# Kernel optimization log

Hardware: AMD Instinct MI355X
Metric: run time of the kernel (lower is better)

The kernel has to match this reference:

```python
import jax, jax.numpy as jnp
import numpy as np

B, C, F, T = 4, 64, 256, 256
CH = C // 2  # self.n_ch inside the module
EPS = 1e-5


def _cbp(x, W, b, g, be, m, v, a):
    # 1x1 conv == channel matmul, then BatchNorm (inference stats) + PReLU (scalar slope)
    y = jnp.einsum('oi,bift->boft', W, x) + b[None, :, None, None]
    y = (y - m[None, :, None, None]) * jax.lax.rsqrt(v[None, :, None, None] + EPS)
    y = y * g[None, :, None, None] + be[None, :, None, None]
    return jnp.where(y > 0, y, a * y)


def setup_inputs() -> dict:
    key = jax.random.key(0)
    ks = jax.random.split(key, 16)

    def conv_params(i, cin, cout, pre):
        W = jax.random.normal(ks[i], (cout, cin), dtype=jnp.float32) * 0.05
        return {
            pre + '_W': W,
            pre + '_b': jnp.zeros((cout,), jnp.float32),
            pre + '_g': jnp.ones((cout,), jnp.float32),
            pre + '_be': jnp.zeros((cout,), jnp.float32),
            pre + '_m': jax.random.normal(ks[i + 1], (cout,), dtype=jnp.float32) * 0.1,
            pre + '_v': jax.random.uniform(ks[i + 2], (cout,), dtype=jnp.float32) + 0.5,
            pre + '_a': jnp.float32(0.25),
        }

    d = {
        'inp': jax.random.normal(ks[12], (B, C, F, T), dtype=jnp.float32),
        'x': jax.random.normal(ks[13], (B, C, F, T), dtype=jnp.float32),
    }
    d.update(conv_params(0, C, 2 * CH, 'fqk'))
    d.update(conv_params(3, C, CH, 'fv'))
    d.update(conv_params(6, C, 2 * CH, 'tqk'))
    d.update(conv_params(9, CH, C, 'proj'))
    return d


def reference(inp, x,
              fqk_W, fqk_b, fqk_g, fqk_be, fqk_m, fqk_v, fqk_a,
              fv_W, fv_b, fv_g, fv_be, fv_m, fv_v, fv_a,
              tqk_W, tqk_b, tqk_g, tqk_be, tqk_m, tqk_v, tqk_a,
              proj_W, proj_b, proj_g, proj_be, proj_m, proj_v, proj_a):
    scale = 1.0 / jnp.sqrt(jnp.float32(CH))

    # frequency attention
    f_qk = _cbp(inp, fqk_W, fqk_b, fqk_g, fqk_be, fqk_m, fqk_v, fqk_a)  # B,2CH,F,T
    vf = _cbp(x, fv_W, fv_b, fv_g, fv_be, fv_m, fv_v, fv_a)             # B,CH,F,T
    r = f_qk.reshape(f_qk.shape[0], CH, 2, F, T)  # 'b (c k) f t -> b c k f t'
    qf, kf = r[:, :, 0], r[:, :, 1]
    f_score = jnp.einsum('bcft,bcyt->btfy', qf, kf) * scale
    f_score = jax.nn.softmax(f_score, axis=-1)
    fout = jnp.einsum('btfy,bcyt->bcft', f_score, vf)

    # time attention (causal mask)
    t_qk = _cbp(inp, tqk_W, tqk_b, tqk_g, tqk_be, tqk_m, tqk_v, tqk_a)
    r = t_qk.reshape(t_qk.shape[0], CH, 2, F, T)
    qt, kt = r[:, :, 0], r[:, :, 1]
    t_score = jnp.einsum('bcft,bcfy->bfty', qt, kt) * scale
    mask = jnp.triu(jnp.ones((T, T), dtype=bool), k=1)  # j - i + 1 with i == j
    neg = -jnp.finfo(t_score.dtype).max
    t_score = jnp.where(mask, neg, t_score)
    t_score = jax.nn.softmax(t_score, axis=-1)
    tout = jnp.einsum('bfty,bcfy->bcft', t_score, fout)

    out = _cbp(tout, proj_W, proj_b, proj_g, proj_be, proj_m, proj_v, proj_a)
    return out + x
```

## Files before the change

kernel.cpp:

```cpp
#include <hip/hip_runtime.h>
#include <hip/hip_bf16.h>

typedef __hip_bfloat16 bf16;
typedef __attribute__((ext_vector_type(8))) short bf16x8;
typedef __attribute__((ext_vector_type(4))) float f32x4;
typedef __attribute__((ext_vector_type(16))) float f32x16;
typedef __attribute__((ext_vector_type(8))) unsigned short u16x8;
typedef __attribute__((ext_vector_type(4))) unsigned int u32x4;
typedef __attribute__((ext_vector_type(2))) unsigned int u32x2;

struct ConvP {
  const float* W; const float* bi; const float* g; const float* be;
  const float* m; const float* v; const float* a;
};

#define QS (0.17677669529663687f * 1.4426950408889634f)

__device__ __forceinline__ unsigned short f2bf(float f) {
  __hip_bfloat16 h = __float2bfloat16(f);
  return __builtin_bit_cast(unsigned short, h);
}
__device__ __forceinline__ float bf2f(unsigned short u) {
  return __uint_as_float(((unsigned)u) << 16);
}
__device__ __forceinline__ float fast_exp2(float x) {
#if __has_builtin(__builtin_amdgcn_exp2f)
  return __builtin_amdgcn_exp2f(x);
#else
  return exp2f(x);
#endif
}

__global__ __launch_bounds__(256, 2) void conv_qkv(
    const float* __restrict__ inp, const float* __restrict__ x,
    ConvP fqk, ConvP fv, ConvP tqk,
    bf16* __restrict__ Qf, bf16* __restrict__ Kf, bf16* __restrict__ Vf,
    bf16* __restrict__ Qt, bf16* __restrict__ Kt)
{
  __shared__ __attribute__((aligned(16))) unsigned short Xb[64 * 260];
  __shared__ __attribute__((aligned(16))) unsigned short S0[256 * 40];
  __shared__ __attribute__((aligned(16))) unsigned short S1[256 * 40];
  __shared__ __attribute__((aligned(8)))  float2 Pc[160];

  const int tid = threadIdx.x;
  const int b = blockIdx.x >> 8;
  const int f = blockIdx.x & 255;
  const size_t gbase = (size_t)b * 64 * 65536 + f * 256;
  const size_t tbase = (size_t)(b * 256 + f) * 8192;

  const int lane = tid & 63;
  const int wid = tid >> 6;
  const int m16 = lane & 15;
  const int quad = lane >> 4;

  if (tid < 160) {
    const ConvP& P = (tid < 64) ? fqk : (tid < 128) ? tqk : fv;
    const int o = (tid < 64) ? tid : (tid < 128) ? tid - 64 : tid - 128;
    float A = P.g[o] * rsqrtf(P.v[o] + 1e-5f);
    float B2 = (P.bi[o] - P.m[o]) * A + P.be[o];
    if (tid < 128 && ((o & 1) == 0)) { A *= QS; B2 *= QS; }
    Pc[tid] = make_float2(A, B2);
  }

  auto load_X = [&](const float* __restrict__ src) {
    #pragma unroll
    for (int r = 0; r < 16; ++r) {
      const int idx = r * 256 + tid;
      const int c = idx >> 6;
      const int t0 = (idx & 63) * 4;
      const float4 v = *(const float4*)(src + gbase + (size_t)c * 65536 + t0);
      unsigned lo = (unsigned)f2bf(v.x) | (((unsigned)f2bf(v.y)) << 16);
      unsigned hi = (unsigned)f2bf(v.z) | (((unsigned)f2bf(v.w)) << 16);
      u32x2 pk = {lo, hi};
      *(u32x2*)&Xb[c * 260 + t0] = pk;
    }
  };

  auto load_A = [&](const float* __restrict__ W, int rowbase, int ks) {
    const float* p = W + (rowbase + m16) * 64 + ks * 32 + quad * 8;
    const float4 lo = *(const float4*)p;
    const float4 hi = *(const float4*)(p + 4);
    bf16x8 r;
    r[0] = (short)f2bf(lo.x); r[1] = (short)f2bf(lo.y);
    r[2] = (short)f2bf(lo.z); r[3] = (short)f2bf(lo.w);
    r[4] = (short)f2bf(hi.x); r[5] = (short)f2bf(hi.y);
    r[6] = (short)f2bf(hi.z); r[7] = (short)f2bf(hi.w);
    return r;
  };

  auto load_B = [&](int tt, int ks) {
    const int t = tt * 16 + m16;
    const int i0 = ks * 32 + quad * 8;
    bf16x8 r;
    #pragma unroll
    for (int j = 0; j < 8; ++j) r[j] = (short)Xb[(i0 + j) * 260 + t];
    return r;
  };

  auto emit = [&](const unsigned short* S, bf16* __restrict__ dst) {
    #pragma unroll
    for (int r = 0; r < 4; ++r) {
      const int chunk = r * 256 + tid;
      const int t = chunk >> 2, part = chunk & 3;
      u32x4 v = *(const u32x4*)&S[t * 40 + part * 8];
      *(u32x4*)(dst + tbase + (size_t)chunk * 8) = v;
    }
  };

  auto leaky = [](float y, float alpha) { return y > 0.f ? y : alpha * y; };

  auto qk_pass = [&](const ConvP& P, int pcb, const bf16x8 (&Bf)[4][2]) {
    bf16x8 A[4][2];
    #pragma unroll
    for (int ot = 0; ot < 4; ++ot)
      #pragma unroll
      for (int ks = 0; ks < 2; ++ks) A[ot][ks] = load_A(P.W, ot * 16, ks);
    float pA[4][4], pB[4][4];
    #pragma unroll
    for (int ot = 0; ot < 4; ++ot)
      #pragma unroll
      for (int r = 0; r < 4; ++r) {
        const float2 pp = Pc[pcb + ot * 16 + quad * 4 + r];
        pA[ot][r] = pp.x; pB[ot][r] = pp.y;
      }
    const float alpha = P.a[0];
    #pragma unroll
    for (int i = 0; i < 4; ++i) {
      const int t = (wid * 4 + i) * 16 + m16;
      #pragma unroll
      for (int ot = 0; ot < 4; ++ot) {
        f32x4 acc = {0.f, 0.f, 0.f, 0.f};
        acc = __builtin_amdgcn_mfma_f32_16x16x32_bf16(A[ot][0], Bf[i][0], acc, 0, 0, 0);
        acc = __builtin_amdgcn_mfma_f32_16x16x32_bf16(A[ot][1], Bf[i][1], acc, 0, 0, 0);
        float y[4];
        #pragma unroll
        for (int r = 0; r < 4; ++r)
          y[r] = leaky(acc[r] * pA[ot][r] + pB[ot][r], alpha);
        const int ch0 = ot * 8 + quad * 2;
        *(unsigned*)&S0[t * 40 + ch0] = (unsigned)f2bf(y[0]) | (((unsigned)f2bf(y[2])) << 16);
        *(unsigned*)&S1[t * 40 + ch0] = (unsigned)f2bf(y[1]) | (((unsigned)f2bf(y[3])) << 16);
      }
    }
  };

  load_X(inp);
  __syncthreads();

  bf16x8 Bf[4][2];
  #pragma unroll
  for (int i = 0; i < 4; ++i)
    #pragma unroll
    for (int ks = 0; ks < 2; ++ks) Bf[i][ks] = load_B(wid * 4 + i, ks);

  qk_pass(fqk, 0, Bf);
  __syncthreads();
  emit(S0, Qf); emit(S1, Kf);
  __syncthreads();
  qk_pass(tqk, 64, Bf);
  __syncthreads();
  emit(S0, Qt); emit(S1, Kt);
  __syncthreads();
  load_X(x);
  __syncthreads();

  {
    bf16x8 A[2][2], Bv[4][2];
    #pragma unroll
    for (int i = 0; i < 4; ++i)
      #pragma unroll
      for (int ks = 0; ks < 2; ++ks) Bv[i][ks] = load_B(wid * 4 + i, ks);
    #pragma unroll
    for (int ot = 0; ot < 2; ++ot)
      #pragma unroll
      for (int ks = 0; ks < 2; ++ks) A[ot][ks] = load_A(fv.W, ot * 16, ks);
    float pA[2][4], pB[2][4];
    #pragma unroll
    for (int ot = 0; ot < 2; ++ot)
      #pragma unroll
      for (int r = 0; r < 4; ++r) {
        const float2 pp = Pc[128 + ot * 16 + quad * 4 + r];
        pA[ot][r] = pp.x; pB[ot][r] = pp.y;
      }
    const float alpha = fv.a[0];
    #pragma unroll
    for (int i = 0; i < 4; ++i) {
      const int t = (wid * 4 + i) * 16 + m16;
      #pragma unroll
      for (int ot = 0; ot < 2; ++ot) {
        f32x4 acc = {0.f, 0.f, 0.f, 0.f};
        acc = __builtin_amdgcn_mfma_f32_16x16x32_bf16(A[ot][0], Bv[i][0], acc, 0, 0, 0);
        acc = __builtin_amdgcn_mfma_f32_16x16x32_bf16(A[ot][1], Bv[i][1], acc, 0, 0, 0);
        float y[4];
        #pragma unroll
        for (int r = 0; r < 4; ++r)
          y[r] = leaky(acc[r] * pA[ot][r] + pB[ot][r], alpha);
        const int ch = ot * 16 + quad * 4;
        *(unsigned*)&S0[t * 40 + ch]     = (unsigned)f2bf(y[0]) | (((unsigned)f2bf(y[1])) << 16);
        *(unsigned*)&S0[t * 40 + ch + 2] = (unsigned)f2bf(y[2]) | (((unsigned)f2bf(y[3])) << 16);
      }
    }
  }
  __syncthreads();
  emit(S0, Vf);
}

template<bool CAUSAL>
__global__ __launch_bounds__(256, 2) void attn_k(
    const bf16* __restrict__ Qg, const bf16* __restrict__ Kg,
    const bf16* __restrict__ Vg, bf16* __restrict__ Og)
{
  __shared__ __attribute__((aligned(16))) unsigned short Kl[256 * 40];
  __shared__ __attribute__((aligned(16))) unsigned short Vt[32 * 264];
  __shared__ __attribute__((aligned(16))) unsigned short Plds[4][16 * 264];
  __shared__ __attribute__((aligned(16))) unsigned short Wsc[4][16 * 40];

  const int inst = blockIdx.x;
  const int b = inst >> 8;
  const int s = inst & 255;
  constexpr int RS = CAUSAL ? 32 : 8192;
  const int qbase = CAUSAL ? inst * 8192 : (b * 2097152 + s * 32);

  const int tid = threadIdx.x;
  #pragma unroll
  for (int k2 = 0; k2 < 4; ++k2) {
    const int chunk = k2 * 256 + tid;
    const int row = chunk >> 2, part = chunk & 3;
    u32x4 val = *(const u32x4*)(Kg + qbase + row * RS + part * 8);
    *(u32x4*)&Kl[row * 40 + part * 8] = val;
  }
  if (tid < 128) {
    const unsigned short* v0 = (const unsigned short*)(Vg + qbase) + (2 * tid) * RS;
    const unsigned short* v1 = v0 + RS;
    u16x8 a[4], c[4];
    #pragma unroll
    for (int q = 0; q < 4; ++q) {
      a[q] = *(const u16x8*)(v0 + 8 * q);
      c[q] = *(const u16x8*)(v1 + 8 * q);
    }
    unsigned int* vt32 = (unsigned int*)Vt;
    #pragma unroll
    for (int cc = 0; cc < 32; ++cc) {
      unsigned lo = a[cc >> 3][cc & 7];
      unsigned hi = c[cc >> 3][cc & 7];
      vt32[(cc * 264 + 2 * tid) >> 1] = lo | (hi << 16);
    }
  }
  __syncthreads();

  const int lane = tid & 63;
  const int wid = tid >> 6;
  const int m16 = lane & 15;
  const int quad = lane >> 4;

  unsigned short* P  = &Plds[wid][0];
  unsigned short* Ws = &Wsc[wid][0];
  const int r4 = lane >> 2, p4 = lane & 3;

  bf16x8 kfr[16];
  #pragma unroll
  for (int ct = 0; ct < 16; ++ct)
    kfr[ct] = *(const bf16x8*)&Kl[(ct * 16 + m16) * 40 + quad * 8];

  #pragma unroll 1
  for (int it = 0; it < 4; ++it) {
    const int rt = wid + 4 * it;
    {
      u32x4 qv = *(const u32x4*)(Qg + qbase + (rt * 16 + r4) * RS + p4 * 8);
      *(u32x4*)&Ws[r4 * 40 + p4 * 8] = qv;
    }
    const bf16x8 qf = *(const bf16x8*)&Ws[m16 * 40 + quad * 8];
    const int nct = CAUSAL ? (rt + 1) : 16;

    f32x4 acc[16];
    #pragma unroll
    for (int ct = 0; ct < 16; ++ct) {
      if (ct < nct) {
        f32x4 z = {0.f, 0.f, 0.f, 0.f};
        acc[ct] = __builtin_amdgcn_mfma_f32_16x16x32_bf16(qf, kfr[ct], z, 0, 0, 0);
      }
    }
    float mx[4] = {-3e38f, -3e38f, -3e38f, -3e38f};
    #pragma unroll
    for (int ct = 0; ct < 16; ++ct) if (ct < nct) {
      #pragma unroll
      for (int r = 0; r < 4; ++r) {
        float v = acc[ct][r];
        if (CAUSAL && (ct == nct - 1) && (m16 > quad * 4 + r)) v = -3e38f;
        acc[ct][r] = v;
        mx[r] = fmaxf(mx[r], v);
      }
    }
    #pragma unroll
    for (int r = 0; r < 4; ++r) {
      float m = mx[r];
      #pragma unroll
      for (int d = 1; d < 16; d <<= 1) m = fmaxf(m, __shfl_xor(m, d, 16));
      mx[r] = m;
    }
    float sum[4] = {0.f, 0.f, 0.f, 0.f};
    #pragma unroll
    for (int ct = 0; ct < 16; ++ct) if (ct < nct) {
      #pragma unroll
      for (int r = 0; r < 4; ++r) {
        float p = fast_exp2(acc[ct][r] - mx[r]);
        acc[ct][r] = p;
        sum[r] += p;
      }
    }
    float inv[4];
    #pragma unroll
    for (int r = 0; r < 4; ++r) {
      float ssum = sum[r];
      #pragma unroll
      for (int d = 1; d < 16; d <<= 1) ssum += __shfl_xor(ssum, d, 16);
      inv[r] = 1.0f / ssum;
    }
    #pragma unroll
    for (int ct = 0; ct < 16; ++ct) if (ct < nct) {
      #pragma unroll
      for (int r = 0; r < 4; ++r)
        P[(quad * 4 + r) * 264 + ct * 16 + m16] = f2bf(acc[ct][r]);
    }
    int ksteps = CAUSAL ? ((rt >> 1) + 1) : 8;
    if (CAUSAL && ((rt & 1) == 0)) {
      #pragma unroll
      for (int u = 0; u < 4; ++u) {
        const int e = lane + 64 * u;
        P[(e >> 4) * 264 + (rt + 1) * 16 + (e & 15)] = 0;
      }
    }
    f32x4 o0 = {0.f, 0.f, 0.f, 0.f}, o1 = {0.f, 0.f, 0.f, 0.f};
    #pragma unroll
    for (int ks = 0; ks < 8; ++ks) {
      if (ks < ksteps) {
        const bf16x8 pf  = *(const bf16x8*)&P[m16 * 264 + ks * 32 + quad * 8];
        const bf16x8 vf0 = *(const bf16x8*)&Vt[m16 * 264 + ks * 32 + quad * 8];
        const bf16x8 vf1 = *(const bf16x8*)&Vt[(16 + m16) * 264 + ks * 32 + quad * 8];
        o0 = __builtin_amdgcn_mfma_f32_16x16x32_bf16(pf, vf0, o0, 0, 0, 0);
        o1 = __builtin_amdgcn_mfma_f32_16x16x32_bf16(pf, vf1, o1, 0, 0, 0);
      }
    }
    #pragma unroll
    for (int r = 0; r < 4; ++r) {
      Ws[(quad * 4 + r) * 40 + m16]      = f2bf(o0[r] * inv[r]);
      Ws[(quad * 4 + r) * 40 + 16 + m16] = f2bf(o1[r] * inv[r]);
    }
    {
      u32x4 ov = *(const u32x4*)&Ws[r4 * 40 + p4 * 8];
      *(u32x4*)(Og + qbase + (rt * 16 + r4) * RS + p4 * 8) = ov;
    }
  }
}

__global__ __launch_bounds__(256) void proj_k(
    const bf16* __restrict__ tout, const float* __restrict__ x,
    ConvP pj, float* __restrict__ out)
{
  __shared__ float2 Pc[64];
  const int tid = threadIdx.x;
  const int b = blockIdx.x >> 8;
  const int f = blockIdx.x & 255;
  if (tid < 64) {
    const float A = pj.g[tid] * rsqrtf(pj.v[tid] + 1e-5f);
    const float B2 = (pj.bi[tid] - pj.m[tid]) * A + pj.be[tid];
    Pc[tid] = make_float2(A, B2);
  }
  const int lane = tid & 63;
  const int wid = tid >> 6;
  const int n32 = lane & 31;
  const int h = lane >> 5;

  bf16x8 Afr[2][2];
  #pragma unroll
  for (int ot = 0; ot < 2; ++ot)
    #pragma unroll
    for (int ks = 0; ks < 2; ++ks) {
      const float* p = pj.W + (ot * 32 + n32) * 32 + ks * 16 + h * 8;
      const float4 lo = *(const float4*)p;
      const float4 hi = *(const float4*)(p + 4);
      bf16x8 r;
      r[0] = (short)f2bf(lo.x); r[1] = (short)f2bf(lo.y);
      r[2] = (short)f2bf(lo.z); r[3] = (short)f2bf(lo.w);
      r[4] = (short)f2bf(hi.x); r[5] = (short)f2bf(hi.y);
      r[6] = (short)f2bf(hi.z); r[7] = (short)f2bf(hi.w);
      Afr[ot][ks] = r;
    }
  __syncthreads();

  const float alpha = pj.a[0];
  const size_t gbase = (size_t)b * 64 * 65536 + f * 256;
  const size_t tbase = (size_t)(b * 256 + f) * 8192;

  #pragma unroll
  for (int tt = 0; tt < 2; ++tt) {
    const int t = wid * 64 + tt * 32 + n32;
    const bf16x8 B0 = *(const bf16x8*)(tout + tbase + (size_t)t * 32 + 0 * 16 + h * 8);
    const bf16x8 B1 = *(const bf16x8*)(tout + tbase + (size_t)t * 32 + 1 * 16 + h * 8);
    #pragma unroll
    for (int ot = 0; ot < 2; ++ot) {
      f32x16 acc = {};
      acc = __builtin_amdgcn_mfma_f32_32x32x16_bf16(Afr[ot][0], B0, acc, 0, 0, 0);
      acc = __builtin_amdgcn_mfma_f32_32x32x16_bf16(Afr[ot][1], B1, acc, 0, 0, 0);
      #pragma unroll
      for (int reg = 0; reg < 16; ++reg) {
        const int o = ot * 32 + (reg & 3) + 8 * (reg >> 2) + 4 * h;
        const float2 pp = Pc[o];
        float y = acc[reg] * pp.x + pp.y;
        y = y > 0.f ? y : alpha * y;
        const size_t off = gbase + (size_t)o * 65536 + t;
        out[off] = y + x[off];
      }
    }
  }
}

extern "C" void kernel_launch(void* const* d_in, const int* in_sizes, int n_in,
                              void* d_out, int out_size, void* d_ws, size_t ws_size,
                              hipStream_t stream) {
  const float* inp = (const float*)d_in[0];
  const float* x   = (const float*)d_in[1];
  auto cp = [&](int i) {
    return ConvP{ (const float*)d_in[i],     (const float*)d_in[i + 1],
                  (const float*)d_in[i + 2], (const float*)d_in[i + 3],
                  (const float*)d_in[i + 4], (const float*)d_in[i + 5],
                  (const float*)d_in[i + 6] };
  };
  ConvP fqk = cp(2), fv = cp(9), tqk = cp(16), pj = cp(23);

  char* ws = (char*)d_ws;
  const size_t SZ = (size_t)4 * 256 * 256 * 32 * 2;
  bf16* Qf = (bf16*)(ws + 0 * SZ);
  bf16* Kf = (bf16*)(ws + 1 * SZ);
  bf16* Vf = (bf16*)(ws + 2 * SZ);
  bf16* Qt = (bf16*)(ws + 3 * SZ);
  bf16* Kt = (bf16*)(ws + 4 * SZ);
  bf16* Ft = (bf16*)(ws + 5 * SZ);
  bf16* To = (bf16*)(ws + 0 * SZ);

  conv_qkv<<<1024, 256, 0, stream>>>(inp, x, fqk, fv, tqk, Qf, Kf, Vf, Qt, Kt);
  attn_k<false><<<1024, 256, 0, stream>>>(Qf, Kf, Vf, Ft);
  attn_k<true><<<1024, 256, 0, stream>>>(Qt, Kt, Ft, To);
  proj_k<<<1024, 256, 0, stream>>>(To, x, pj, (float*)d_out);
}
```

Before: 329.9 us.

## Shrink LDS footprint to raise occupancy in conv and attention kernels

The conv kernel now splits each (b,f) row into two half-T blocks, which halves its shared-memory tiles and doubles the grid. Its launch bound is raised to 4 blocks per CU. In the attention kernel, K is stored in shared memory as an XOR-swizzled unpadded tile, and only half the K fragments are kept in registers; the rest are reloaded from shared memory. P is staged in two 128-column halves, which reuses its buffer as the Q/output scratch and drops the separate Ws array. Together these cut LDS use and register pressure so 3 blocks per CU can fit. The cost is extra LDS reads for K, more loop control, and redundant parameter setup in the conv kernel.

```diff
diff --git a/kernel.cpp b/kernel.cpp
--- a/kernel.cpp
+++ b/kernel.cpp
@@ -31,22 +31,23 @@
 #endif
 }
 
-__global__ __launch_bounds__(256, 2) void conv_qkv(
+__global__ __launch_bounds__(256, 4) void conv_qkv(
     const float* __restrict__ inp, const float* __restrict__ x,
     ConvP fqk, ConvP fv, ConvP tqk,
     bf16* __restrict__ Qf, bf16* __restrict__ Kf, bf16* __restrict__ Vf,
     bf16* __restrict__ Qt, bf16* __restrict__ Kt)
 {
-  __shared__ __attribute__((aligned(16))) unsigned short Xb[64 * 260];
-  __shared__ __attribute__((aligned(16))) unsigned short S0[256 * 40];
-  __shared__ __attribute__((aligned(16))) unsigned short S1[256 * 40];
+  __shared__ __attribute__((aligned(16))) unsigned short Xb[64 * 132];
+  __shared__ __attribute__((aligned(16))) unsigned short S0[128 * 40];
+  __shared__ __attribute__((aligned(16))) unsigned short S1[128 * 40];
   __shared__ __attribute__((aligned(8)))  float2 Pc[160];
 
   const int tid = threadIdx.x;
-  const int b = blockIdx.x >> 8;
-  const int f = blockIdx.x & 255;
-  const size_t gbase = (size_t)b * 64 * 65536 + f * 256;
-  const size_t tbase = (size_t)(b * 256 + f) * 8192;
+  const int th = blockIdx.x & 1;
+  const int f = (blockIdx.x >> 1) & 255;
+  const int b = blockIdx.x >> 9;
+  const size_t gbase = (size_t)b * 64 * 65536 + f * 256 + th * 128;
+  const size_t tbase = (size_t)(b * 256 + f) * 8192 + th * 4096;
 
   const int lane = tid & 63;
   const int wid = tid >> 6;
@@ -64,15 +65,15 @@
 
   auto load_X = [&](const float* __restrict__ src) {
     #pragma unroll
-    for (int r = 0; r < 16; ++r) {
+    for (int r = 0; r < 8; ++r) {
       const int idx = r * 256 + tid;
-      const int c = idx >> 6;
-      const int t0 = (idx & 63) * 4;
+      const int c = idx >> 5;
+      const int t0 = (idx & 31) * 4;
       const float4 v = *(const float4*)(src + gbase + (size_t)c * 65536 + t0);
       unsigned lo = (unsigned)f2bf(v.x) | (((unsigned)f2bf(v.y)) << 16);
       unsigned hi = (unsigned)f2bf(v.z) | (((unsigned)f2bf(v.w)) << 16);
       u32x2 pk = {lo, hi};
-      *(u32x2*)&Xb[c * 260 + t0] = pk;
+      *(u32x2*)&Xb[c * 132 + t0] = pk;
     }
   };
 
@@ -93,13 +94,13 @@
     const int i0 = ks * 32 + quad * 8;
     bf16x8 r;
     #pragma unroll
-    for (int j = 0; j < 8; ++j) r[j] = (short)Xb[(i0 + j) * 260 + t];
+    for (int j = 0; j < 8; ++j) r[j] = (short)Xb[(i0 + j) * 132 + t];
     return r;
   };
 
   auto emit = [&](const unsigned short* S, bf16* __restrict__ dst) {
     #pragma unroll
-    for (int r = 0; r < 4; ++r) {
+    for (int r = 0; r < 2; ++r) {
       const int chunk = r * 256 + tid;
       const int t = chunk >> 2, part = chunk & 3;
       u32x4 v = *(const u32x4*)&S[t * 40 + part * 8];
@@ -109,7 +110,7 @@
 
   auto leaky = [](float y, float alpha) { return y > 0.f ? y : alpha * y; };
 
-  auto qk_pass = [&](const ConvP& P, int pcb, const bf16x8 (&Bf)[4][2]) {
+  auto qk_pass = [&](const ConvP& P, int pcb, const bf16x8 (&Bf)[2][2]) {
     bf16x8 A[4][2];
     #pragma unroll
     for (int ot = 0; ot < 4; ++ot)
@@ -125,8 +126,8 @@
       }
     const float alpha = P.a[0];
     #pragma unroll
-    for (int i = 0; i < 4; ++i) {
-      const int t = (wid * 4 + i) * 16 + m16;
+    for (int i = 0; i < 2; ++i) {
+      const int t = (wid * 2 + i) * 16 + m16;
       #pragma unroll
       for (int ot = 0; ot < 4; ++ot) {
         f32x4 acc = {0.f, 0.f, 0.f, 0.f};
@@ -146,11 +147,11 @@
   load_X(inp);
   __syncthreads();
 
-  bf16x8 Bf[4][2];
+  bf16x8 Bf[2][2];
   #pragma unroll
-  for (int i = 0; i < 4; ++i)
-    #pragma unroll
-    for (int ks = 0; ks < 2; ++ks) Bf[i][ks] = load_B(wid * 4 + i, ks);
+  for (int i = 0; i < 2; ++i)
+    #pragma unroll
+    for (int ks = 0; ks < 2; ++ks) Bf[i][ks] = load_B(wid * 2 + i, ks);
 
   qk_pass(fqk, 0, Bf);
   __syncthreads();
@@ -164,11 +165,11 @@
   __syncthreads();
 
   {
-    bf16x8 A[2][2], Bv[4][2];
-    #pragma unroll
-    for (int i = 0; i < 4; ++i)
-      #pragma unroll
-      for (int ks = 0; ks < 2; ++ks) Bv[i][ks] = load_B(wid * 4 + i, ks);
+    bf16x8 A[2][2], Bv[2][2];
+    #pragma unroll
+    for (int i = 0; i < 2; ++i)
+      #pragma unroll
+      for (int ks = 0; ks < 2; ++ks) Bv[i][ks] = load_B(wid * 2 + i, ks);
     #pragma unroll
     for (int ot = 0; ot < 2; ++ot)
       #pragma unroll
@@ -183,8 +184,8 @@
       }
     const float alpha = fv.a[0];
     #pragma unroll
-    for (int i = 0; i < 4; ++i) {
-      const int t = (wid * 4 + i) * 16 + m16;
+    for (int i = 0; i < 2; ++i) {
+      const int t = (wid * 2 + i) * 16 + m16;
       #pragma unroll
       for (int ot = 0; ot < 2; ++ot) {
         f32x4 acc = {0.f, 0.f, 0.f, 0.f};
@@ -205,14 +206,13 @@
 }
 
 template<bool CAUSAL>
-__global__ __launch_bounds__(256, 2) void attn_k(
+__global__ __launch_bounds__(256, 3) void attn_k(
     const bf16* __restrict__ Qg, const bf16* __restrict__ Kg,
     const bf16* __restrict__ Vg, bf16* __restrict__ Og)
 {
-  __shared__ __attribute__((aligned(16))) unsigned short Kl[256 * 40];
+  __shared__ __attribute__((aligned(16))) unsigned short Kl[256 * 32];
   __shared__ __attribute__((aligned(16))) unsigned short Vt[32 * 264];
-  __shared__ __attribute__((aligned(16))) unsigned short Plds[4][16 * 264];
-  __shared__ __attribute__((aligned(16))) unsigned short Wsc[4][16 * 40];
+  __shared__ __attribute__((aligned(16))) unsigned short Plds[4][16 * 136];
 
   const int inst = blockIdx.x;
   const int b = inst >> 8;
@@ -226,7 +226,7 @@
     const int chunk = k2 * 256 + tid;
     const int row = chunk >> 2, part = chunk & 3;
     u32x4 val = *(const u32x4*)(Kg + qbase + row * RS + part * 8);
-    *(u32x4*)&Kl[row * 40 + part * 8] = val;
+    *(u32x4*)&Kl[row * 32 + ((part ^ (row & 3)) * 8)] = val;
   }
   if (tid < 128) {
     const unsigned short* v0 = (const unsigned short*)(Vg + qbase) + (2 * tid) * RS;
@@ -252,23 +252,23 @@
   const int m16 = lane & 15;
   const int quad = lane >> 4;
 
-  unsigned short* P  = &Plds[wid][0];
-  unsigned short* Ws = &Wsc[wid][0];
+  unsigned short* P = &Plds[wid][0];
   const int r4 = lane >> 2, p4 = lane & 3;
-
-  bf16x8 kfr[16];
+  const int ksw = (quad ^ (m16 & 3)) * 8;
+
+  bf16x8 kfr[8];
   #pragma unroll
-  for (int ct = 0; ct < 16; ++ct)
-    kfr[ct] = *(const bf16x8*)&Kl[(ct * 16 + m16) * 40 + quad * 8];
+  for (int ct = 0; ct < 8; ++ct)
+    kfr[ct] = *(const bf16x8*)&Kl[(ct * 16 + m16) * 32 + ksw];
 
   #pragma unroll 1
   for (int it = 0; it < 4; ++it) {
     const int rt = wid + 4 * it;
     {
       u32x4 qv = *(const u32x4*)(Qg + qbase + (rt * 16 + r4) * RS + p4 * 8);
-      *(u32x4*)&Ws[r4 * 40 + p4 * 8] = qv;
-    }
-    const bf16x8 qf = *(const bf16x8*)&Ws[m16 * 40 + quad * 8];
+      *(u32x4*)&P[r4 * 40 + p4 * 8] = qv;
+    }
+    const bf16x8 qf = *(const bf16x8*)&P[m16 * 40 + quad * 8];
     const int nct = CAUSAL ? (rt + 1) : 16;
 
     f32x4 acc[16];
@@ -276,7 +276,9 @@
     for (int ct = 0; ct < 16; ++ct) {
       if (ct < nct) {
         f32x4 z = {0.f, 0.f, 0.f, 0.f};
-        acc[ct] = __builtin_amdgcn_mfma_f32_16x16x32_bf16(qf, kfr[ct], z, 0, 0, 0);
+        const bf16x8 kf = (ct < 8) ? kfr[ct]
+            : *(const bf16x8*)&Kl[(ct * 16 + m16) * 32 + ksw];
+        acc[ct] = __builtin_amdgcn_mfma_f32_16x16x32_bf16(qf, kf, z, 0, 0, 0);
       }
     }
     float mx[4] = {-3e38f, -3e38f, -3e38f, -3e38f};
@@ -315,38 +317,48 @@
       for (int d = 1; d < 16; d <<= 1) ssum += __shfl_xor(ssum, d, 16);
       inv[r] = 1.0f / ssum;
     }
-    #pragma unroll
-    for (int ct = 0; ct < 16; ++ct) if (ct < nct) {
-      #pragma unroll
-      for (int r = 0; r < 4; ++r)
-        P[(quad * 4 + r) * 264 + ct * 16 + m16] = f2bf(acc[ct][r]);
-    }
-    int ksteps = CAUSAL ? ((rt >> 1) + 1) : 8;
-    if (CAUSAL && ((rt & 1) == 0)) {
-      #pragma unroll
-      for (int u = 0; u < 4; ++u) {
-        const int e = lane + 64 * u;
-        P[(e >> 4) * 264 + (rt + 1) * 16 + (e & 15)] = 0;
-      }
-    }
+    const int ksteps = CAUSAL ? ((rt >> 1) + 1) : 8;
     f32x4 o0 = {0.f, 0.f, 0.f, 0.f}, o1 = {0.f, 0.f, 0.f, 0.f};
     #pragma unroll
-    for (int ks = 0; ks < 8; ++ks) {
-      if (ks < ksteps) {
-        const bf16x8 pf  = *(const bf16x8*)&P[m16 * 264 + ks * 32 + quad * 8];
-        const bf16x8 vf0 = *(const bf16x8*)&Vt[m16 * 264 + ks * 32 + quad * 8];
-        const bf16x8 vf1 = *(const bf16x8*)&Vt[(16 + m16) * 264 + ks * 32 + quad * 8];
-        o0 = __builtin_amdgcn_mfma_f32_16x16x32_bf16(pf, vf0, o0, 0, 0, 0);
-        o1 = __builtin_amdgcn_mfma_f32_16x16x32_bf16(pf, vf1, o1, 0, 0, 0);
+    for (int h = 0; h < 2; ++h) {
+      if (!CAUSAL || (8 * h) < nct) {
+        #pragma unroll
+        for (int c2 = 0; c2 < 8; ++c2) {
+          const int ct = 8 * h + c2;
+          if (ct < nct) {
+            #pragma unroll
+            for (int r = 0; r < 4; ++r)
+              P[(quad * 4 + r) * 136 + c2 * 16 + m16] = f2bf(acc[ct][r]);
+          }
+        }
+        if (CAUSAL && ((rt & 1) == 0) && (((rt + 1) >> 3) == h)) {
+          const int cl = rt + 1 - 8 * h;
+          #pragma unroll
+          for (int u = 0; u < 4; ++u) {
+            const int e = lane + 64 * u;
+            P[(e >> 4) * 136 + cl * 16 + (e & 15)] = 0;
+          }
+        }
+        #pragma unroll
+        for (int k4 = 0; k4 < 4; ++k4) {
+          const int ks = 4 * h + k4;
+          if (ks < ksteps) {
+            const bf16x8 pf  = *(const bf16x8*)&P[m16 * 136 + k4 * 32 + quad * 8];
+            const bf16x8 vf0 = *(const bf16x8*)&Vt[m16 * 264 + ks * 32 + quad * 8];
+            const bf16x8 vf1 = *(const bf16x8*)&Vt[(16 + m16) * 264 + ks * 32 + quad * 8];
+            o0 = __builtin_amdgcn_mfma_f32_16x16x32_bf16(pf, vf0, o0, 0, 0, 0);
+            o1 = __builtin_amdgcn_mfma_f32_16x16x32_bf16(pf, vf1, o1, 0, 0, 0);
+          }
+        }
       }
     }
     #pragma unroll
     for (int r = 0; r < 4; ++r) {
-      Ws[(quad * 4 + r) * 40 + m16]      = f2bf(o0[r] * inv[r]);
-      Ws[(quad * 4 + r) * 40 + 16 + m16] = f2bf(o1[r] * inv[r]);
+      P[(quad * 4 + r) * 40 + m16]      = f2bf(o0[r] * inv[r]);
+      P[(quad * 4 + r) * 40 + 16 + m16] = f2bf(o1[r] * inv[r]);
     }
     {
-      u32x4 ov = *(const u32x4*)&Ws[r4 * 40 + p4 * 8];
+      u32x4 ov = *(const u32x4*)&P[r4 * 40 + p4 * 8];
       *(u32x4*)(Og + qbase + (rt * 16 + r4) * RS + p4 * 8) = ov;
     }
   }
@@ -437,7 +449,7 @@
   bf16* Ft = (bf16*)(ws + 5 * SZ);
   bf16* To = (bf16*)(ws + 0 * SZ);
 
-  conv_qkv<<<1024, 256, 0, stream>>>(inp, x, fqk, fv, tqk, Qf, Kf, Vf, Qt, Kt);
+  conv_qkv<<<2048, 256, 0, stream>>>(inp, x, fqk, fv, tqk, Qf, Kf, Vf, Qt, Kt);
   attn_k<false><<<1024, 256, 0, stream>>>(Qf, Kf, Vf, Ft);
   attn_k<true><<<1024, 256, 0, stream>>>(Qt, Kt, Ft, To);
   proj_k<<<1024, 256, 0, stream>>>(To, x, pj, (float*)d_out);
```

Result: slower. 349.8 us (+6.1%).
